# Kernel optimization log

Measured on AMD Instinct MI355X. Metric: run time of the kernel, lower is better.

Reference implementation:

```python
import jax, jax.numpy as jnp
import numpy as np

TOP_K = 6
N_EXPERTS = 64
ALPHA = 1e-3


def setup_inputs() -> dict:
    key = jax.random.key(0)
    k1, k2 = jax.random.split(key)
    bsz, seq_len, h = 4, 4096, 2048
    hidden_states = jax.random.normal(k1, (bsz, seq_len, h), dtype=jnp.float32)
    # kaiming_uniform_(a=sqrt(5)) on [E, h] -> bound = 1/sqrt(h)
    bound = 1.0 / np.sqrt(h)
    weight = jax.random.uniform(k2, (N_EXPERTS, h), dtype=jnp.float32, minval=-bound, maxval=bound)
    return {"hidden_states": hidden_states, "weight": weight}


def reference(hidden_states, weight):
    bsz, seq_len, h = hidden_states.shape
    E = weight.shape[0]
    x = hidden_states.reshape(-1, h)                      # [T, h], T = bsz*seq_len
    logits = jnp.einsum('th,eh->te', x, weight)           # router linear (no bias)
    scores = jax.nn.softmax(logits, axis=-1)              # [T, E]
    topk_weight, topk_idx = jax.lax.top_k(scores, TOP_K)  # [T, K]
    # norm_topk_prob renormalization
    topk_weight = topk_weight / (jnp.sum(topk_weight, axis=-1, keepdims=True) + 1e-20)
    # seq_aux auxiliary load-balancing loss (training path)
    idx_b = topk_idx.reshape(bsz, seq_len * TOP_K)        # [B, S*K]
    ce = jnp.sum(jax.nn.one_hot(idx_b, E, dtype=scores.dtype), axis=1)  # [B, E] counts
    ce = ce / (seq_len * TOP_K / E)
    mean_scores = scores.reshape(bsz, seq_len, E).mean(axis=1)          # [B, E]
    aux_loss = jnp.mean(jnp.sum(ce * mean_scores, axis=1)) * ALPHA
    return topk_idx, topk_weight, aux_loss
```

## Files before the change

### kernel.cpp

```cpp
#include <hip/hip_runtime.h>
#include <math.h>

#pragma clang fp contract(off)

#define T_TOKENS 16384
#define HDIM 2048
#define NEXP 64
#define TOPK 6
#define SEQ 4096
#define TPB 32
#define KC 64
#define WS 68
#define XS 68
#define LGS 65
#define PS 65

__device__ __forceinline__ void np_upd(const float4& w0, const float4& w1,
                                       const float4& w2, const float4& w3,
                                       const float4& x0, const float4& x1,
                                       const float4& x2, const float4& x3,
                                       float acc[4])
{
    acc[0] = w0.x*x0.x + (w1.x*x1.x + (w2.x*x2.x + (w3.x*x3.x + acc[0])));
    acc[1] = w0.y*x0.y + (w1.y*x1.y + (w2.y*x2.y + (w3.y*x3.y + acc[1])));
    acc[2] = w0.z*x0.z + (w1.z*x1.z + (w2.z*x2.z + (w3.z*x3.z + acc[2])));
    acc[3] = w0.w*x0.w + (w1.w*x1.w + (w2.w*x2.w + (w3.w*x3.w + acc[3])));
}

__global__ __launch_bounds__(512, 4) void moe_gate_main(
    const float* __restrict__ x, const float* __restrict__ wgt,
    float* __restrict__ out, float* __restrict__ gacc)
{
    __shared__ float w_lds[NEXP * WS];
    __shared__ float x_lds[TPB * XS];
    __shared__ float lg[TPB * LGS];
    __shared__ float probs[TPB * PS];
    __shared__ float psum[8 * NEXP];
    __shared__ int   cnt[NEXP];

    const int tid  = threadIdx.x;
    const int bid  = blockIdx.x;
    const int tb   = bid * TPB;
    const int b    = tb / SEQ;

    const int lane = tid & 63;
    const int wv   = tid >> 6;
    const int le   = lane & 15;
    const int g    = lane >> 4;
    const int trow = wv * 4 + g;

    float acc[4][4];
    #pragma unroll
    for (int j = 0; j < 4; ++j)
        #pragma unroll
        for (int l = 0; l < 4; ++l) acc[j][l] = 0.f;

    for (int c = 0; c < HDIM / KC; ++c) {
        const int k0 = c * KC;
        #pragma unroll
        for (int i = 0; i < 2; ++i) {
            int idx = i * 512 + tid;
            int e = idx >> 4, c4 = idx & 15;
            float4 v = *reinterpret_cast<const float4*>(&wgt[e * HDIM + k0 + c4 * 4]);
            *reinterpret_cast<float4*>(&w_lds[e * WS + c4 * 4]) = v;
        }
        {
            int t = tid >> 4, c4 = tid & 15;
            float4 v = *reinterpret_cast<const float4*>(&x[(size_t)(tb + t) * HDIM + k0 + c4 * 4]);
            *reinterpret_cast<float4*>(&x_lds[t * XS + c4 * 4]) = v;
        }
        __syncthreads();

        #pragma unroll
        for (int b16 = 0; b16 < 4; ++b16) {
            const int kb = b16 * 16;
            float4 xa[4];
            #pragma unroll
            for (int j = 0; j < 4; ++j)
                xa[j] = *reinterpret_cast<const float4*>(&x_lds[trow * XS + kb + j * 4]);
            #pragma unroll
            for (int je = 0; je < 4; ++je) {
                const float* wr = &w_lds[(le + 16 * je) * WS + kb];
                float4 w0 = *reinterpret_cast<const float4*>(wr);
                float4 w1 = *reinterpret_cast<const float4*>(wr + 4);
                float4 w2 = *reinterpret_cast<const float4*>(wr + 8);
                float4 w3 = *reinterpret_cast<const float4*>(wr + 12);
                np_upd(w0, w1, w2, w3, xa[0], xa[1], xa[2], xa[3], acc[je]);
            }
        }
        __syncthreads();
    }

    #pragma unroll
    for (int je = 0; je < 4; ++je) {
        float v = (acc[je][0] + acc[je][1]) + (acc[je][2] + acc[je][3]);
        lg[trow * LGS + le + 16 * je] = v;
    }
    if (tid < NEXP) cnt[tid] = 0;
    __syncthreads();

    if (tid < TPB) {
        const int t = tid;
        float mx = lg[t * LGS];
        for (int e = 1; e < NEXP; ++e) { float v = lg[t * LGS + e]; if (v > mx) mx = v; }
        for (int e = 0; e < NEXP; ++e)
            probs[t * PS + e] = expf(lg[t * LGS + e] - mx);
        float r[8];
        #pragma unroll
        for (int j = 0; j < 8; ++j) r[j] = probs[t * PS + j];
        for (int i = 8; i < 64; i += 8)
            #pragma unroll
            for (int j = 0; j < 8; ++j) r[j] += probs[t * PS + i + j];
        float S = ((r[0] + r[1]) + (r[2] + r[3])) + ((r[4] + r[5]) + (r[6] + r[7]));
        for (int e = 0; e < NEXP; ++e) probs[t * PS + e] = probs[t * PS + e] / S;
    }
    __syncthreads();

    {
        const int e = tid & 63, q = tid >> 6;
        float s = 0.f;
        for (int t = q * 4; t < q * 4 + 4; ++t) s += probs[t * PS + e];
        psum[q * 64 + e] = s;
    }
    __syncthreads();

    if (tid < TPB) {
        const int t = tid;
        const int gt = tb + t;
        float pv[TOPK]; int pi[TOPK];
        for (int r = 0; r < TOPK; ++r) {
            float bv = -1.f; int be = 0;
            for (int e = 0; e < NEXP; ++e) {
                float v = probs[t * PS + e];
                if (v > bv) { bv = v; be = e; }
            }
            probs[t * PS + be] = -1.f;
            pv[r] = bv; pi[r] = be;
            atomicAdd(&cnt[be], 1);
        }
        float wsum = pv[0];
        #pragma unroll
        for (int r = 1; r < TOPK; ++r) wsum += pv[r];
        wsum += 1e-20f;
        #pragma unroll
        for (int r = 0; r < TOPK; ++r) {
            out[(size_t)gt * TOPK + r] = (float)pi[r];
            out[(size_t)T_TOKENS * TOPK + (size_t)gt * TOPK + r] = pv[r] / wsum;
        }
    } else if (tid >= 64 && tid < 128) {
        const int e = tid - 64;
        float s = 0.f;
        #pragma unroll
        for (int q = 0; q < 8; ++q) s += psum[q * 64 + e];
        atomicAdd(&gacc[b * 64 + e], s);
    }
    __syncthreads();
    if (tid < NEXP) {
        atomicAdd(&gacc[256 + b * 64 + tid], (float)cnt[tid]);
    }
}

__global__ __launch_bounds__(256) void moe_gate_aux(
    const float* __restrict__ gacc, float* __restrict__ out)
{
    __shared__ float red[4];
    const int tid = threadIdx.x;
    float v = gacc[256 + tid] * gacc[tid];
    #pragma unroll
    for (int o = 32; o > 0; o >>= 1) v += __shfl_down(v, o, 64);
    if ((tid & 63) == 0) red[tid >> 6] = v;
    __syncthreads();
    if (tid == 0) {
        float tot = red[0] + red[1] + red[2] + red[3];
        const float scale = (64.0f / (4096.0f * 6.0f)) / 4096.0f;
        out[2 * T_TOKENS * TOPK] = 1e-3f * (tot * scale) * 0.25f;
    }
}

extern "C" void kernel_launch(void* const* d_in, const int* in_sizes, int n_in,
                              void* d_out, int out_size, void* d_ws, size_t ws_size,
                              hipStream_t stream) {
    const float* x   = (const float*)d_in[0];
    const float* wgt = (const float*)d_in[1];
    float* out  = (float*)d_out;
    float* gacc = (float*)d_ws;

    hipMemsetAsync(d_ws, 0, 512 * sizeof(float), stream);
    moe_gate_main<<<T_TOKENS / TPB, 512, 0, stream>>>(x, wgt, out, gacc);
    moe_gate_aux<<<1, 256, 0, stream>>>(gacc, out);
}
```

Measured before the change: 305.2 us.

## Stream x via async LDS double buffer and read weights as wave-uniform scalars

```diff
diff --git a/kernel.cpp b/kernel.cpp
--- a/kernel.cpp
+++ b/kernel.cpp
@@ -8,46 +8,49 @@
 #define NEXP 64
 #define TOPK 6
 #define SEQ 4096
-#define TPB 32
+#define TPB 64
 #define KC 64
-#define WS 68
-#define XS 68
+#define NC (HDIM / KC)
 #define LGS 65
 #define PS 65
 
-__device__ __forceinline__ void np_upd(const float4& w0, const float4& w1,
-                                       const float4& w2, const float4& w3,
-                                       const float4& x0, const float4& x1,
-                                       const float4& x2, const float4& x3,
-                                       float acc[4])
+typedef __attribute__((ext_vector_type(16))) float f32x16;
+typedef __attribute__((address_space(1))) const unsigned int gu32;
+typedef __attribute__((address_space(3))) unsigned int lu32;
+
+__device__ __forceinline__ void np_upd16(const f32x16 w,
+                                         const float4& x0, const float4& x1,
+                                         const float4& x2, const float4& x3,
+                                         float acc[4])
 {
-    acc[0] = w0.x*x0.x + (w1.x*x1.x + (w2.x*x2.x + (w3.x*x3.x + acc[0])));
-    acc[1] = w0.y*x0.y + (w1.y*x1.y + (w2.y*x2.y + (w3.y*x3.y + acc[1])));
-    acc[2] = w0.z*x0.z + (w1.z*x1.z + (w2.z*x2.z + (w3.z*x3.z + acc[2])));
-    acc[3] = w0.w*x0.w + (w1.w*x1.w + (w2.w*x2.w + (w3.w*x3.w + acc[3])));
+    acc[0] = w[0]*x0.x + (w[4]*x1.x + (w[8]*x2.x  + (w[12]*x3.x + acc[0])));
+    acc[1] = w[1]*x0.y + (w[5]*x1.y + (w[9]*x2.y  + (w[13]*x3.y + acc[1])));
+    acc[2] = w[2]*x0.z + (w[6]*x1.z + (w[10]*x2.z + (w[14]*x3.z + acc[2])));
+    acc[3] = w[3]*x0.w + (w[7]*x1.w + (w[11]*x2.w + (w[15]*x3.w + acc[3])));
 }
 
-__global__ __launch_bounds__(512, 4) void moe_gate_main(
+__global__ __launch_bounds__(1024, 4) void moe_gate_main(
     const float* __restrict__ x, const float* __restrict__ wgt,
     float* __restrict__ out, float* __restrict__ gacc)
 {
-    __shared__ float w_lds[NEXP * WS];
-    __shared__ float x_lds[TPB * XS];
+    __shared__ __attribute__((aligned(16))) float xs[2 * TPB * KC];
     __shared__ float lg[TPB * LGS];
     __shared__ float probs[TPB * PS];
-    __shared__ float psum[8 * NEXP];
+    __shared__ float psum[16 * NEXP];
     __shared__ int   cnt[NEXP];
 
     const int tid  = threadIdx.x;
     const int bid  = blockIdx.x;
     const int tb   = bid * TPB;
-    const int b    = tb / SEQ;
+    const int b    = bid >> 6;
 
     const int lane = tid & 63;
-    const int wv   = tid >> 6;
-    const int le   = lane & 15;
-    const int g    = lane >> 4;
-    const int trow = wv * 4 + g;
+    const int e0   = __builtin_amdgcn_readfirstlane(tid >> 6) * 4;
+
+    const int srow = tid >> 4;
+    const int ss   = (tid & 15) ^ (srow & 7);
+    const float* xsrc = x + (size_t)(tb + srow) * HDIM + ss * 4;
+    char* ldst = (char*)xs + tid * 16;
 
     float acc[4][4];
     #pragma unroll
@@ -55,37 +58,32 @@
         #pragma unroll
         for (int l = 0; l < 4; ++l) acc[j][l] = 0.f;
 
-    for (int c = 0; c < HDIM / KC; ++c) {
-        const int k0 = c * KC;
-        #pragma unroll
-        for (int i = 0; i < 2; ++i) {
-            int idx = i * 512 + tid;
-            int e = idx >> 4, c4 = idx & 15;
-            float4 v = *reinterpret_cast<const float4*>(&wgt[e * HDIM + k0 + c4 * 4]);
-            *reinterpret_cast<float4*>(&w_lds[e * WS + c4 * 4]) = v;
-        }
-        {
-            int t = tid >> 4, c4 = tid & 15;
-            float4 v = *reinterpret_cast<const float4*>(&x[(size_t)(tb + t) * HDIM + k0 + c4 * 4]);
-            *reinterpret_cast<float4*>(&x_lds[t * XS + c4 * 4]) = v;
-        }
-        __syncthreads();
+    __builtin_amdgcn_global_load_lds((gu32*)xsrc, (lu32*)ldst, 16, 0, 0);
+    __syncthreads();
 
+    const char* xrow = (const char*)xs + lane * (KC * 4);
+    const int   swz  = lane & 7;
+
+    for (int c = 0; c < NC; ++c) {
+        const int cur = c & 1;
+        if (c + 1 < NC)
+            __builtin_amdgcn_global_load_lds((gu32*)(xsrc + (c + 1) * KC),
+                                             (lu32*)(ldst + ((cur ^ 1) * TPB * KC * 4)),
+                                             16, 0, 0);
+
+        const char* xb = xrow + cur * (TPB * KC * 4);
+        const float* wc = wgt + (size_t)e0 * HDIM + c * KC;
         #pragma unroll
         for (int b16 = 0; b16 < 4; ++b16) {
-            const int kb = b16 * 16;
-            float4 xa[4];
-            #pragma unroll
-            for (int j = 0; j < 4; ++j)
-                xa[j] = *reinterpret_cast<const float4*>(&x_lds[trow * XS + kb + j * 4]);
+            const float4 xa0 = *(const float4*)(xb + (((b16 * 4 + 0) ^ swz) << 4));
+            const float4 xa1 = *(const float4*)(xb + (((b16 * 4 + 1) ^ swz) << 4));
+            const float4 xa2 = *(const float4*)(xb + (((b16 * 4 + 2) ^ swz) << 4));
+            const float4 xa3 = *(const float4*)(xb + (((b16 * 4 + 3) ^ swz) << 4));
             #pragma unroll
             for (int je = 0; je < 4; ++je) {
-                const float* wr = &w_lds[(le + 16 * je) * WS + kb];
-                float4 w0 = *reinterpret_cast<const float4*>(wr);
-                float4 w1 = *reinterpret_cast<const float4*>(wr + 4);
-                float4 w2 = *reinterpret_cast<const float4*>(wr + 8);
-                float4 w3 = *reinterpret_cast<const float4*>(wr + 12);
-                np_upd(w0, w1, w2, w3, xa[0], xa[1], xa[2], xa[3], acc[je]);
+                const f32x16 w = *reinterpret_cast<const f32x16*>(
+                    wc + (size_t)je * HDIM + b16 * 16);
+                np_upd16(w, xa0, xa1, xa2, xa3, acc[je]);
             }
         }
         __syncthreads();
@@ -94,7 +92,7 @@
     #pragma unroll
     for (int je = 0; je < 4; ++je) {
         float v = (acc[je][0] + acc[je][1]) + (acc[je][2] + acc[je][3]);
-        lg[trow * LGS + le + 16 * je] = v;
+        lg[lane * LGS + e0 + je] = v;
     }
     if (tid < NEXP) cnt[tid] = 0;
     __syncthreads();
@@ -151,7 +149,7 @@
         const int e = tid - 64;
         float s = 0.f;
         #pragma unroll
-        for (int q = 0; q < 8; ++q) s += psum[q * 64 + e];
+        for (int q = 0; q < 16; ++q) s += psum[q * 64 + e];
         atomicAdd(&gacc[b * 64 + e], s);
     }
     __syncthreads();
@@ -186,6 +184,6 @@
     float* gacc = (float*)d_ws;
 
     hipMemsetAsync(d_ws, 0, 512 * sizeof(float), stream);
-    moe_gate_main<<<T_TOKENS / TPB, 512, 0, stream>>>(x, wgt, out, gacc);
+    moe_gate_main<<<T_TOKENS / TPB, 1024, 0, stream>>>(x, wgt, out, gacc);
     moe_gate_aux<<<1, 256, 0, stream>>>(gacc, out);
 }
```

Measured after the change: 388.0 us. 1.27x slower.

## Double-buffer GEMV tiles with direct global-to-LDS loads and XOR swizzle

Applied to the files above, without the earlier changes.

```diff
diff --git a/kernel.cpp b/kernel.cpp
--- a/kernel.cpp
+++ b/kernel.cpp
@@ -10,10 +10,12 @@
 #define SEQ 4096
 #define TPB 32
 #define KC 64
-#define WS 68
-#define XS 68
+#define NC (HDIM / KC)
 #define LGS 65
 #define PS 65
+
+typedef __attribute__((address_space(1))) const unsigned int gu32;
+typedef __attribute__((address_space(3))) unsigned int lu32;
 
 __device__ __forceinline__ void np_upd(const float4& w0, const float4& w1,
                                        const float4& w2, const float4& w3,
@@ -31,8 +33,8 @@
     const float* __restrict__ x, const float* __restrict__ wgt,
     float* __restrict__ out, float* __restrict__ gacc)
 {
-    __shared__ float w_lds[NEXP * WS];
-    __shared__ float x_lds[TPB * XS];
+    __shared__ __attribute__((aligned(16))) float w_lds[2][NEXP * KC];
+    __shared__ __attribute__((aligned(16))) float x_lds[2][TPB * KC];
     __shared__ float lg[TPB * LGS];
     __shared__ float probs[TPB * PS];
     __shared__ float psum[8 * NEXP];
@@ -49,42 +51,58 @@
     const int g    = lane >> 4;
     const int trow = wv * 4 + g;
 
+    const int wrow0 = tid >> 4;
+    const int wp    = tid & 15;
+    const int wls   = wp ^ (wrow0 & 7);
+    const float* wgsrc0 = wgt + (size_t)wrow0 * HDIM + wls * 4;
+    const float* wgsrc1 = wgt + (size_t)(wrow0 + 32) * HDIM + wls * 4;
+    const int xrow = tid >> 4;
+    const int xls  = (tid & 15) ^ (xrow & 7);
+    const float* xgsrc = x + (size_t)(tb + xrow) * HDIM + xls * 4;
+    char* wdst0 = (char*)&w_lds[0][0] + tid * 16;
+    char* wdst1 = wdst0 + 512 * 16;
+    char* xdst  = (char*)&x_lds[0][0] + tid * 16;
+
     float acc[4][4];
     #pragma unroll
     for (int j = 0; j < 4; ++j)
         #pragma unroll
         for (int l = 0; l < 4; ++l) acc[j][l] = 0.f;
 
-    for (int c = 0; c < HDIM / KC; ++c) {
-        const int k0 = c * KC;
-        #pragma unroll
-        for (int i = 0; i < 2; ++i) {
-            int idx = i * 512 + tid;
-            int e = idx >> 4, c4 = idx & 15;
-            float4 v = *reinterpret_cast<const float4*>(&wgt[e * HDIM + k0 + c4 * 4]);
-            *reinterpret_cast<float4*>(&w_lds[e * WS + c4 * 4]) = v;
-        }
-        {
-            int t = tid >> 4, c4 = tid & 15;
-            float4 v = *reinterpret_cast<const float4*>(&x[(size_t)(tb + t) * HDIM + k0 + c4 * 4]);
-            *reinterpret_cast<float4*>(&x_lds[t * XS + c4 * 4]) = v;
-        }
-        __syncthreads();
-
+    __builtin_amdgcn_global_load_lds((gu32*)wgsrc0, (lu32*)wdst0, 16, 0, 0);
+    __builtin_amdgcn_global_load_lds((gu32*)wgsrc1, (lu32*)wdst1, 16, 0, 0);
+    __builtin_amdgcn_global_load_lds((gu32*)xgsrc,  (lu32*)xdst,  16, 0, 0);
+    __syncthreads();
+
+    const int xswz = trow & 7;
+    const int wswz = le & 7;
+
+    for (int c = 0; c < NC; ++c) {
+        const int cur = c & 1;
+        if (c + 1 < NC) {
+            const int k1 = (c + 1) * KC;
+            const int bo_w = (cur ^ 1) * (NEXP * KC * 4);
+            const int bo_x = (cur ^ 1) * (TPB * KC * 4);
+            __builtin_amdgcn_global_load_lds((gu32*)(wgsrc0 + k1), (lu32*)(wdst0 + bo_w), 16, 0, 0);
+            __builtin_amdgcn_global_load_lds((gu32*)(wgsrc1 + k1), (lu32*)(wdst1 + bo_w), 16, 0, 0);
+            __builtin_amdgcn_global_load_lds((gu32*)(xgsrc  + k1), (lu32*)(xdst  + bo_x), 16, 0, 0);
+        }
+
+        const char* wb = (const char*)&w_lds[cur][0];
+        const char* xb = (const char*)&x_lds[cur][0] + trow * 256;
         #pragma unroll
         for (int b16 = 0; b16 < 4; ++b16) {
-            const int kb = b16 * 16;
             float4 xa[4];
             #pragma unroll
             for (int j = 0; j < 4; ++j)
-                xa[j] = *reinterpret_cast<const float4*>(&x_lds[trow * XS + kb + j * 4]);
+                xa[j] = *(const float4*)(xb + (((b16 * 4 + j) ^ xswz) << 4));
             #pragma unroll
             for (int je = 0; je < 4; ++je) {
-                const float* wr = &w_lds[(le + 16 * je) * WS + kb];
-                float4 w0 = *reinterpret_cast<const float4*>(wr);
-                float4 w1 = *reinterpret_cast<const float4*>(wr + 4);
-                float4 w2 = *reinterpret_cast<const float4*>(wr + 8);
-                float4 w3 = *reinterpret_cast<const float4*>(wr + 12);
+                const char* wr = wb + (le + 16 * je) * 256;
+                const float4 w0 = *(const float4*)(wr + (((b16 * 4 + 0) ^ wswz) << 4));
+                const float4 w1 = *(const float4*)(wr + (((b16 * 4 + 1) ^ wswz) << 4));
+                const float4 w2 = *(const float4*)(wr + (((b16 * 4 + 2) ^ wswz) << 4));
+                const float4 w3 = *(const float4*)(wr + (((b16 * 4 + 3) ^ wswz) << 4));
                 np_upd(w0, w1, w2, w3, xa[0], xa[1], xa[2], xa[3], acc[je]);
             }
         }
```

Measured after the change: 336.1 us. +10.2%, slower.
